# Kernel optimization log

Measured on AMD Instinct MI355X. Metric: run time of the kernel, lower is better.

## Reference

```python
import jax, jax.numpy as jnp
import numpy as np

N = 50000      # nodes
E = 800000     # edges (before self-loops)
F_IN = 256     # feature_size
H = 96         # hidden_channels
G = 64         # graphs in batch
NC = 4         # num_classes
EPS = 1e-5     # BatchNorm eps


def _lrelu(x, s=0.01):
    return jnp.where(x >= 0, x, s * x)


def _gat(x, W, a_s, a_d, b, src, dst):
    # PyG GATConv, heads=1: linear transform, edge-wise LeakyReLU(0.2) scores,
    # segment softmax over destination nodes, scatter-add aggregation.
    h = x @ W                                                  # [N,H]
    e = _lrelu((h * a_s).sum(-1)[src] + (h * a_d).sum(-1)[dst], 0.2)  # [E+N]
    m = jax.ops.segment_max(e, dst, num_segments=N)
    ee = jnp.exp(e - m[dst])
    denom = jax.ops.segment_sum(ee, dst, num_segments=N)
    alpha = ee / denom[dst]
    return jax.ops.segment_sum(alpha[:, None] * h[src], dst, num_segments=N) + b


def _bn(x, g, b):
    # training-mode BatchNorm over the node dimension
    mu = x.mean(0)
    var = ((x - mu) ** 2).mean(0)
    return g * (x - mu) / jnp.sqrt(var + EPS) + b


def setup_inputs() -> dict:
    key = jax.random.key(0)
    ks = jax.random.split(key, 20)
    p = lambda i, sh: jax.random.normal(ks[i], sh, jnp.float32) * 0.05
    inp = {
        "x": jax.random.normal(ks[0], (N, F_IN), jnp.float32),
        "edge_index": jax.random.randint(ks[1], (2, E), 0, N),
        "batch": jnp.sort(jax.random.randint(ks[2], (N,), 0, G)),
        "embed_W": p(3, (F_IN, H)), "embed_b": jnp.zeros((H,), jnp.float32),
        "conv1_W": p(4, (H, H)), "conv1_as": p(5, (H,)), "conv1_ad": p(6, (H,)), "conv1_b": jnp.zeros((H,), jnp.float32),
        "conv2_W": p(7, (H, H)), "conv2_as": p(8, (H,)), "conv2_ad": p(9, (H,)), "conv2_b": jnp.zeros((H,), jnp.float32),
        "conv3_W": p(10, (H, H)), "conv3_as": p(11, (H,)), "conv3_ad": p(12, (H,)), "conv3_b": jnp.zeros((H,), jnp.float32),
        "fc1_W": p(13, (H, H)), "fc1_b": jnp.zeros((H,), jnp.float32),
        "fc2_W": p(14, (H, H)), "fc2_b": jnp.zeros((H,), jnp.float32),
        "bn1_g": jnp.ones((H,), jnp.float32), "bn1_b": jnp.zeros((H,), jnp.float32),
        "bn2_g": jnp.ones((H,), jnp.float32), "bn2_b": jnp.zeros((H,), jnp.float32),
        "bn3_g": jnp.ones((H,), jnp.float32), "bn3_b": jnp.zeros((H,), jnp.float32),
        "fc3_W": p(15, (H, H // 2)), "fc3_b": jnp.zeros((H // 2,), jnp.float32),
        "fc4_W": p(16, (H // 2, NC)), "fc4_b": jnp.zeros((NC,), jnp.float32),
    }
    return inp


def reference(x, edge_index, batch, embed_W, embed_b,
              conv1_W, conv1_as, conv1_ad, conv1_b,
              conv2_W, conv2_as, conv2_ad, conv2_b,
              conv3_W, conv3_as, conv3_ad, conv3_b,
              fc1_W, fc1_b, fc2_W, fc2_b,
              bn1_g, bn1_b, bn2_g, bn2_b, bn3_g, bn3_b,
              fc3_W, fc3_b, fc4_W, fc4_b):
    loops = jnp.arange(N)
    src = jnp.concatenate([edge_index[0], loops])   # GATConv add_self_loops=True
    dst = jnp.concatenate([edge_index[1], loops])

    h = _lrelu(x @ embed_W + embed_b)
    identity = h
    h = _lrelu(_bn(_gat(h, conv1_W, conv1_as, conv1_ad, conv1_b, src, dst), bn1_g, bn1_b)) + identity
    h = _lrelu(h @ fc1_W + fc1_b)
    h = _lrelu(_bn(_gat(h, conv2_W, conv2_as, conv2_ad, conv2_b, src, dst), bn2_g, bn2_b)) + identity
    h = _lrelu(h @ fc2_W + fc2_b)
    h = _lrelu(_bn(_gat(h, conv3_W, conv3_as, conv3_ad, conv3_b, src, dst), bn3_g, bn3_b)) + identity

    # Poincare ball expmap0 with c=1: tanh(||u||) * u / ||u||
    n = jnp.maximum(jnp.linalg.norm(h, axis=-1, keepdims=True), 1e-15)
    h = jnp.tanh(n) * h / n

    cnt = jax.ops.segment_sum(jnp.ones((N,), h.dtype), batch, num_segments=G)
    pooled = jax.ops.segment_sum(h, batch, num_segments=G) / jnp.maximum(cnt, 1.0)[:, None]

    o = _lrelu(pooled @ fc3_W + fc3_b)
    return o @ fc4_W + fc4_b
```

## Files before the change

### kernel.cpp

```cpp
#include <hip/hip_runtime.h>
#include <hip/hip_bf16.h>

#define DEVINL __device__ __forceinline__

constexpr int N_NODES = 50000;
constexpr int N_EDGES = 800000;
constexpr int F_IN    = 256;
constexpr int H       = 96;
constexpr int NG      = 64;
constexpr float BN_EPS = 1e-5f;
constexpr int SLOT    = 64;
constexpr int NREP    = 8;
constexpr int REPSZ   = NG * H + NG;

typedef short bf16x8 __attribute__((ext_vector_type(8)));
typedef float f32x4  __attribute__((ext_vector_type(4)));

DEVINL float bf2f(unsigned int u) {
    union { unsigned int i; float f; } c; c.i = u << 16; return c.f;
}
DEVINL unsigned short f2bf(float f) {
    union { float f; unsigned int i; } c; c.f = f;
    unsigned int x = c.i;
    return (unsigned short)((x + 0x7fffu + ((x >> 16) & 1u)) >> 16);
}
DEVINL float lrelu01(float v) { return v >= 0.f ? v : 0.01f * v; }
DEVINL float ldf(const void* p, size_t i, int f32) {
    return f32 ? ((const float*)p)[i] : bf2f(((const unsigned short*)p)[i]);
}

__global__ __launch_bounds__(256) void detect_fill_k(const unsigned short* __restrict__ x,
                                                     int* __restrict__ flag,
                                                     int* __restrict__ fill)
{
    if (blockIdx.x == 0 && threadIdx.x < 64) {
        int l = threadIdx.x;
        float f = bf2f(x[l]);
        bool huge = !(fabsf(f) <= 1e4f);
        unsigned long long m = __ballot(huge);
        if (l == 0) flag[0] = (__popcll(m) >= 8) ? 1 : 0;
    }
    int i = blockIdx.x * 256 + threadIdx.x;
    if (i < N_NODES) fill[i] = 0;
}

__global__ __launch_bounds__(256) void wpackall_k(
    const void* __restrict__ sE, const void* __restrict__ s0,
    const void* __restrict__ s1, const void* __restrict__ s2,
    const void* __restrict__ s3, const void* __restrict__ s4,
    const int* __restrict__ dflag,
    unsigned short* __restrict__ dE, unsigned short* __restrict__ d0,
    unsigned short* __restrict__ d1, unsigned short* __restrict__ d2,
    unsigned short* __restrict__ d3, unsigned short* __restrict__ d4)
{
    int b = blockIdx.x;
    const void* src; unsigned short* dst; int K, i0;
    if (b < 96) { src = sE; dst = dE; K = F_IN; i0 = b * 256; }
    else {
        int m = (b - 96) / 36, r = (b - 96) % 36;
        K = H; i0 = r * 256;
        if      (m == 0) { src = s0; dst = d0; }
        else if (m == 1) { src = s1; dst = d1; }
        else if (m == 2) { src = s2; dst = d2; }
        else if (m == 3) { src = s3; dst = d3; }
        else             { src = s4; dst = d4; }
    }
    int i = i0 + threadIdx.x;
    if (i >= K * 96) return;
    int c   = i / 3072;
    int rem = i - c * 3072;
    int t    = rem >> 9;
    int rem2 = rem & 511;
    int l = rem2 >> 3, j = rem2 & 7;
    int k = c * 32 + (l >> 4) * 8 + j;
    int n = t * 16 + (l & 15);
    if (dflag[0]) dst[i] = f2bf(((const float*)src)[k * 96 + n]);
    else          dst[i] = ((const unsigned short*)src)[k * 96 + n];
}

template<int EPI, int AWS, int SD, int ABN, int SCAT>
__global__ __launch_bounds__(256) void mgemm_k(
    const void* __restrict__ Ap, const unsigned short* __restrict__ Wpk,
    const void* __restrict__ bp, const int* __restrict__ dflag,
    unsigned short* __restrict__ out, unsigned short* __restrict__ out2,
    const void* __restrict__ as_, const void* __restrict__ ad_,
    float* __restrict__ s, float* __restrict__ d,
    const float* __restrict__ coefp, const unsigned short* __restrict__ idn,
    const int* __restrict__ ei, int* __restrict__ fill,
    unsigned short* __restrict__ colw, int e0, int e1, int ngb,
    int M, int K)
{
    if (SCAT && (int)blockIdx.x >= ngb) {
        int e = e0 + ((int)blockIdx.x - ngb) * 256 + threadIdx.x;
        if (e < e1) {
            int srcv = ei[e];
            int dstv = ei[N_EDGES + e];
            int p = atomicAdd(&fill[dstv], 1);
            if (p < SLOT) colw[(size_t)dstv * SLOT + p] = (unsigned short)srcv;
        }
        return;
    }

    const int f32  = AWS ? 0 : dflag[0];
    const int wf32 = dflag[0];
    const int l    = threadIdx.x & 63;
    const int wave = threadIdx.x >> 6;
    const int row0 = blockIdx.x * 64 + wave * 16;
    const int m    = l & 15;
    const int q    = l >> 4;
    const int arow = row0 + m;
    const bool aok = arow < M;

    f32x4 acc[6] = {};
    const int nch = K >> 5;
    const bf16x8* wp = (const bf16x8*)Wpk;

    for (int c = 0; c < nch; c++) {
        bf16x8 a = {};
        if (aok) {
            if (ABN) {
                const int f0 = c * 32 + q * 8;
                uint4 xu = *(const uint4*)((const unsigned short*)Ap + (size_t)arow * K + f0);
                uint4 iu = *(const uint4*)(idn + (size_t)arow * K + f0);
                unsigned int xs[4] = { xu.x, xu.y, xu.z, xu.w };
                unsigned int is[4] = { iu.x, iu.y, iu.z, iu.w };
                #pragma unroll
                for (int jj = 0; jj < 4; jj++) {
                    int f = f0 + 2 * jj;
                    float v0 = lrelu01(bf2f(xs[jj] & 0xffff) * coefp[f]     + coefp[96 + f])     + bf2f(is[jj] & 0xffff);
                    float v1 = lrelu01(bf2f(xs[jj] >> 16)    * coefp[f + 1] + coefp[96 + f + 1]) + bf2f(is[jj] >> 16);
                    a[2 * jj]     = (short)f2bf(v0);
                    a[2 * jj + 1] = (short)f2bf(v1);
                }
            } else if (f32) {
                const float* A = (const float*)Ap + (size_t)arow * K + c * 32 + q * 8;
                #pragma unroll
                for (int j = 0; j < 8; j++) a[j] = (short)f2bf(A[j]);
            } else {
                a = *(const bf16x8*)((const unsigned short*)Ap + (size_t)arow * K + c * 32 + q * 8);
            }
        }
        const int base = c * 384 + l;
        #pragma unroll
        for (int t = 0; t < 6; t++)
            acc[t] = __builtin_amdgcn_mfma_f32_16x16x32_bf16(a, wp[base + t * 64], acc[t], 0, 0, 0);
    }

    float bv[6];
    if (EPI > 0) {
        #pragma unroll
        for (int t = 0; t < 6; t++) bv[t] = ldf(bp, t * 16 + m, wf32);
    }
    #pragma unroll
    for (int r = 0; r < 4; r++) {
        int rr = row0 + q * 4 + r;
        if (rr >= M) continue;
        size_t o = (size_t)rr * 96 + m;
        #pragma unroll
        for (int t = 0; t < 6; t++) {
            float v = acc[t][r];
            if (EPI > 0) v = lrelu01(v + bv[t]);
            unsigned short sv = f2bf(v);
            out[o + t * 16] = sv;
            if (EPI == 2) out2[o + t * 16] = sv;
        }
    }

    if (SD) {
        float asv[6], adv[6];
        #pragma unroll
        for (int t = 0; t < 6; t++) {
            asv[t] = ldf(as_, t * 16 + m, wf32);
            adv[t] = ldf(ad_, t * 16 + m, wf32);
        }
        #pragma unroll
        for (int r = 0; r < 4; r++) {
            float ps = 0.f, pd = 0.f;
            #pragma unroll
            for (int t = 0; t < 6; t++) {
                ps = fmaf(acc[t][r], asv[t], ps);
                pd = fmaf(acc[t][r], adv[t], pd);
            }
            #pragma unroll
            for (int off = 1; off < 16; off <<= 1) {
                ps += __shfl_xor(ps, off);
                pd += __shfl_xor(pd, off);
            }
            int rr = row0 + q * 4 + r;
            if (m == 0 && rr < M) { s[rr] = ps; d[rr] = pd; }
        }
    }
}

__global__ __launch_bounds__(256) void agg_k(
    const unsigned short* __restrict__ h2, const float* __restrict__ s,
    const float* __restrict__ d, const int* __restrict__ fill,
    const unsigned short* __restrict__ col, const void* __restrict__ bias,
    const int* __restrict__ dflag, unsigned short* __restrict__ out,
    float* __restrict__ bnsum, float* __restrict__ zp, int M)
{
    __shared__ uint2 uwb[4][80];
    if (blockIdx.x == 0 && threadIdx.x < 192) bnsum[threadIdx.x] = 0.f;
    if (zp) {
        int zi = blockIdx.x * 256 + threadIdx.x;
        if (zi < NREP * REPSZ) zp[zi] = 0.f;
    }
    int f32 = dflag[0];
    int v = (blockIdx.x * blockDim.x + threadIdx.x) >> 6;
    int l = threadIdx.x & 63;
    int wv = threadIdx.x >> 6;
    if (v >= M) return;
    int st   = v * SLOT;
    int degr = min(fill[v], SLOT - 1);
    int deg  = degr + 1;

    float dv = d[v];
    int u = 0; float e = -1e30f;
    if (l < degr) {
        u = col[st + l];
        float t = s[u] + dv;
        e = t >= 0.f ? t : 0.2f * t;
    } else if (l == degr) {
        u = v;
        float t = s[v] + dv;
        e = t >= 0.f ? t : 0.2f * t;
    }
    float lm = e;
    #pragma unroll
    for (int off = 32; off > 0; off >>= 1) lm = fmaxf(lm, __shfl_xor(lm, off));
    float w = (l < deg) ? __expf(e - lm) : 0.f;
    float ls = w;
    #pragma unroll
    for (int off = 32; off > 0; off >>= 1) ls += __shfl_xor(ls, off);
    float rden = 1.0f / ls;

    uwb[wv][l] = make_uint2((unsigned int)u, __float_as_uint(w));
    if (l < 16) uwb[wv][64 + l] = make_uint2(0u, 0u);

    bool hw = (l < 48);
    int  c2 = 2 * l;
    float a0 = 0.f, a1 = 0.f;
    const uint2* myuw = uwb[wv];
    for (int j = 0; j < deg; j += 16) {
        uint2 p[16];
        #pragma unroll
        for (int k = 0; k < 16; k++) p[k] = myuw[j + k];
        if (hw) {
            unsigned int hv[16];
            #pragma unroll
            for (int k = 0; k < 16; k++)
                hv[k] = *(const unsigned int*)(h2 + (size_t)p[k].x * 96 + c2);
            #pragma unroll
            for (int k = 0; k < 16; k++) {
                float wj = __uint_as_float(p[k].y);
                a0 = fmaf(wj, bf2f(hv[k] & 0xffff), a0);
                a1 = fmaf(wj, bf2f(hv[k] >> 16),    a1);
            }
        }
    }
    if (hw) {
        float b0 = ldf(bias, c2,     f32);
        float b1 = ldf(bias, c2 + 1, f32);
        unsigned int o = (unsigned int)f2bf(a0 * rden + b0)
                       | ((unsigned int)f2bf(a1 * rden + b1) << 16);
        *(unsigned int*)(out + (size_t)v * 96 + c2) = o;
    }
}

__global__ __launch_bounds__(192) void bnstats_k(const unsigned short* __restrict__ x,
                                                 float* __restrict__ sums, int M)
{
    int c  = threadIdx.x % 96;
    int g2 = threadIdx.x / 96;
    float s = 0.f, q = 0.f;
    for (int r = blockIdx.x * 2 + g2; r < M; r += gridDim.x * 2) {
        float v = bf2f(x[(size_t)r * 96 + c]);
        s += v; q += v * v;
    }
    __shared__ float lsd[192], lqd[192];
    lsd[threadIdx.x] = s; lqd[threadIdx.x] = q;
    __syncthreads();
    if (g2 == 0) {
        atomicAdd(&sums[c],      s + lsd[threadIdx.x + 96]);
        atomicAdd(&sums[96 + c], q + lqd[threadIdx.x + 96]);
    }
}

__global__ void bncoef_k(const float* __restrict__ sums,
                         const void* __restrict__ g_,
                         const void* __restrict__ b_,
                         const int* __restrict__ dflag,
                         float* __restrict__ coef)
{
    int c = threadIdx.x;
    if (c >= 96) return;
    int f32 = dflag[0];
    float mu  = sums[c] * (1.f / N_NODES);
    float var = sums[96 + c] * (1.f / N_NODES) - mu * mu;
    float rinv = 1.0f / sqrtf(var + BN_EPS);
    float sc = ldf(g_, c, f32) * rinv;
    coef[c]      = sc;
    coef[96 + c] = ldf(b_, c, f32) - mu * sc;
}

__global__ __launch_bounds__(256) void bnpool_k(
    const unsigned short* __restrict__ h, const float* __restrict__ coef,
    const unsigned short* __restrict__ iden, const int* __restrict__ batch,
    float* __restrict__ pooled8, int M)
{
    int w = (blockIdx.x * blockDim.x + threadIdx.x) >> 6;
    int l = threadIdx.x & 63;
    int v0 = w * 16;
    if (v0 >= M) return;
    float* P = pooled8 + (blockIdx.x & (NREP - 1)) * REPSZ;
    float* C = P + NG * H;
    bool hw = (l < 48);
    int  c2 = 2 * l;
    float sc0 = 0.f, sc1 = 0.f, sh0 = 0.f, sh1 = 0.f;
    if (hw) {
        sc0 = coef[c2]; sc1 = coef[c2 + 1];
        sh0 = coef[96 + c2]; sh1 = coef[97 + c2];
    }
    int nv = min(16, M - v0);

    int gb[16];
    #pragma unroll
    for (int k = 0; k < 16; k++) gb[k] = batch[v0 + min(k, nv - 1)];

    float x0[16], x1[16], q[16];
    #pragma unroll
    for (int k = 0; k < 16; k++) { x0[k] = 0.f; x1[k] = 0.f; q[k] = 0.f; }
    if (hw) {
        unsigned int xu[16], iu[16];
        #pragma unroll
        for (int k = 0; k < 16; k++) {
            int v = v0 + k;
            if (k < nv) {
                xu[k] = *(const unsigned int*)(h    + (size_t)v * 96 + c2);
                iu[k] = *(const unsigned int*)(iden + (size_t)v * 96 + c2);
            } else { xu[k] = 0u; iu[k] = 0u; }
        }
        #pragma unroll
        for (int k = 0; k < 16; k++) {
            x0[k] = lrelu01(bf2f(xu[k] & 0xffff) * sc0 + sh0) + bf2f(iu[k] & 0xffff);
            x1[k] = lrelu01(bf2f(xu[k] >> 16)    * sc1 + sh1) + bf2f(iu[k] >> 16);
            q[k]  = x0[k] * x0[k] + x1[k] * x1[k];
        }
    }

    #pragma unroll
    for (int off = 32; off > 0; off >>= 1) {
        #pragma unroll
        for (int k = 0; k < 16; k++) q[k] += __shfl_xor(q[k], off);
    }

    float f[16];
    #pragma unroll
    for (int k = 0; k < 16; k++) {
        float n = fmaxf(sqrtf(q[k]), 1e-15f);
        if (n < 15.f) {
            float t = __expf(2.f * n);
            f[k] = (t - 1.f) / ((t + 1.f) * n);
        } else {
            f[k] = 1.f / n;
        }
    }

    float a0 = 0.f, a1 = 0.f, cnt = 0.f;
    int curg = -1;
    for (int k = 0; k < nv; k++) {
        int g = gb[k];
        if (g != curg) {
            if (curg >= 0) {
                if (hw) {
                    atomicAdd(&P[curg * 96 + c2],     a0);
                    atomicAdd(&P[curg * 96 + c2 + 1], a1);
                }
                if (l == 0) atomicAdd(&C[curg], cnt);
            }
            a0 = a1 = 0.f; cnt = 0.f; curg = g;
        }
        a0 = fmaf(f[k], x0[k], a0);
        a1 = fmaf(f[k], x1[k], a1);
        cnt += 1.f;
    }
    if (curg >= 0) {
        if (hw) {
            atomicAdd(&P[curg * 96 + c2],     a0);
            atomicAdd(&P[curg * 96 + c2 + 1], a1);
        }
        if (l == 0) atomicAdd(&C[curg], cnt);
    }
}

__global__ __launch_bounds__(64) void head_k(const float* __restrict__ pooled8,
                                             const void* __restrict__ w3,
                                             const void* __restrict__ b3,
                                             const void* __restrict__ w4,
                                             const void* __restrict__ b4,
                                             const int* __restrict__ dflag,
                                             void* __restrict__ outv)
{
    int g = blockIdx.x;
    int t = threadIdx.x;
    int f32 = dflag[0];
    __shared__ float p[96];
    __shared__ float o[48];
    float cs = 0.f;
    #pragma unroll
    for (int r = 0; r < NREP; r++) cs += pooled8[r * REPSZ + NG * H + g];
    float inv = 1.0f / fmaxf(cs, 1.0f);
    for (int c = t; c < 96; c += 64) {
        float v = 0.f;
        #pragma unroll
        for (int r = 0; r < NREP; r++) v += pooled8[r * REPSZ + g * 96 + c];
        p[c] = v * inv;
    }
    __syncthreads();
    if (t < 48) {
        float a = ldf(b3, t, f32);
        #pragma unroll
        for (int c = 0; c < 96; c++) a = fmaf(p[c], ldf(w3, (size_t)c * 48 + t, f32), a);
        o[t] = lrelu01(a);
    }
    __syncthreads();
    if (t < 4) {
        float a = ldf(b4, t, f32);
        #pragma unroll
        for (int j = 0; j < 48; j++) a = fmaf(o[j], ldf(w4, j * 4 + t, f32), a);
        if (f32) ((float*)outv)[g * 4 + t] = a;
        else     ((unsigned short*)outv)[g * 4 + t] = f2bf(a);
    }
}

extern "C" void kernel_launch(void* const* d_in, const int* in_sizes, int n_in,
                              void* d_out, int out_size, void* d_ws, size_t ws_size,
                              hipStream_t stream)
{
    const void* x     = d_in[0];
    const int*  ei    = (const int*)d_in[1];
    const int*  batch = (const int*)d_in[2];
    const void* embW  = d_in[3];
    const void* embB  = d_in[4];
    const void* convW[3]  = { d_in[5],  d_in[9],  d_in[13] };
    const void* convAs[3] = { d_in[6],  d_in[10], d_in[14] };
    const void* convAd[3] = { d_in[7],  d_in[11], d_in[15] };
    const void* convB[3]  = { d_in[8],  d_in[12], d_in[16] };
    const void* fcW[2]    = { d_in[17], d_in[19] };
    const void* fcB[2]    = { d_in[18], d_in[20] };
    const void* bnG[3]    = { d_in[21], d_in[23], d_in[25] };
    const void* bnB[3]    = { d_in[22], d_in[24], d_in[26] };
    const void* fc3W = d_in[27];
    const void* fc3b = d_in[28];
    const void* fc4W = d_in[29];
    const void* fc4b = d_in[30];

    char* wp_ = (char*)d_ws;
    auto alloc = [&](size_t b) { char* p = wp_; wp_ += (b + 255) & ~(size_t)255; return p; };
    int*   dflag = (int*)alloc(256);
    unsigned short* ident = (unsigned short*)alloc((size_t)N_NODES * H * 2);
    unsigned short* hA    = (unsigned short*)alloc((size_t)N_NODES * H * 2);
    unsigned short* hB    = (unsigned short*)alloc((size_t)N_NODES * H * 2);
    float* s_sc  = (float*)alloc((size_t)N_NODES * 4);
    float* d_sc  = (float*)alloc((size_t)N_NODES * 4);
    float* bnsum = (float*)alloc(192 * 4);
    float* coef  = (float*)alloc(192 * 4);
    float* pooled8 = (float*)alloc((size_t)NREP * REPSZ * 4);
    int*   fill  = (int*)alloc((size_t)N_NODES * 4);
    unsigned short* col = (unsigned short*)alloc((size_t)N_NODES * SLOT * 2);
    unsigned short* wpkEmb = (unsigned short*)alloc((size_t)F_IN * 96 * 2);
    unsigned short* wpkS[5];
    for (int i = 0; i < 5; i++) wpkS[i] = (unsigned short*)alloc((size_t)H * 96 * 2);

    const int GM = (N_NODES + 63) / 64;
    const int GW = (N_NODES * 64 + 255) / 256;
    const int GP = ((N_NODES + 15) / 16 * 64 + 255) / 256;
    const int GF = (N_NODES + 255) / 256;
    const int EH = N_EDGES / 2;
    const int GS = (EH + 255) / 256;

    detect_fill_k<<<GF, 256, 0, stream>>>((const unsigned short*)x, dflag, fill);

    wpackall_k<<<276, 256, 0, stream>>>(embW, convW[0], convW[1], convW[2], fcW[0], fcW[1],
                                        dflag, wpkEmb, wpkS[0], wpkS[1], wpkS[2], wpkS[3], wpkS[4]);

    mgemm_k<2, 0, 0, 0, 1><<<GM + GS, 256, 0, stream>>>(
        x, wpkEmb, embB, dflag, hA, ident,
        nullptr, nullptr, nullptr, nullptr, nullptr, nullptr,
        ei, fill, col, 0, EH, GM, N_NODES, F_IN);

    unsigned short* hcur = hA;
    unsigned short* htmp = hB;

    for (int l = 0; l < 3; l++) {
        if (l == 0) {
            mgemm_k<0, 1, 1, 0, 1><<<GM + GS, 256, 0, stream>>>(
                hcur, wpkS[0], nullptr, dflag, htmp, nullptr,
                convAs[0], convAd[0], s_sc, d_sc, nullptr, nullptr,
                ei, fill, col, EH, N_EDGES, GM, N_NODES, H);
        } else {
            mgemm_k<0, 1, 1, 0, 0><<<GM, 256, 0, stream>>>(
                hcur, wpkS[l], nullptr, dflag, htmp, nullptr,
                convAs[l], convAd[l], s_sc, d_sc, nullptr, nullptr,
                nullptr, nullptr, nullptr, 0, 0, GM, N_NODES, H);
        }
        agg_k<<<GW, 256, 0, stream>>>(htmp, s_sc, d_sc, fill, col, convB[l], dflag, hcur,
                                      bnsum, (l == 2) ? pooled8 : nullptr, N_NODES);
        bnstats_k<<<512, 192, 0, stream>>>(hcur, bnsum, N_NODES);
        bncoef_k<<<1, 128, 0, stream>>>(bnsum, bnG[l], bnB[l], dflag, coef);
        if (l < 2) {
            mgemm_k<1, 1, 0, 1, 0><<<GM, 256, 0, stream>>>(
                hcur, wpkS[3 + l], fcB[l], dflag, htmp, nullptr,
                nullptr, nullptr, nullptr, nullptr, coef, ident,
                nullptr, nullptr, nullptr, 0, 0, GM, N_NODES, H);
            unsigned short* t = hcur; hcur = htmp; htmp = t;
        }
    }

    bnpool_k<<<GP, 256, 0, stream>>>(hcur, coef, ident, batch, pooled8, N_NODES);
    head_k<<<NG, 64, 0, stream>>>(pooled8, fc3W, fc3b, fc4W, fc4b, dflag, d_out);
}
```

Measured before the change: 436.2 us.

## Stage packed weights in LDS, preload A chunks, batch edge scatter per thread

The GEMM kernel now takes K as a template parameter, copies the packed weight matrix into shared memory once per block, and preloads every A chunk into registers before running the MFMA loop. The edge-scatter blocks each handle 8 edges per thread so that loads and atomics are batched. The embedding GEMM writes only to ident (EPI 1), dropping the duplicate hA output, and layer 0 reads from ident. The cost is more LDS per block (48KB for K=256) and more register pressure, which may lower occupancy.

```diff
diff --git a/kernel.cpp b/kernel.cpp
--- a/kernel.cpp
+++ b/kernel.cpp
@@ -12,6 +12,8 @@
 constexpr int SLOT    = 64;
 constexpr int NREP    = 8;
 constexpr int REPSZ   = NG * H + NG;
+constexpr int EPB     = 8;
+constexpr int ECHUNK  = 256 * EPB;
 
 typedef short bf16x8 __attribute__((ext_vector_type(8)));
 typedef float f32x4  __attribute__((ext_vector_type(4)));
@@ -78,7 +80,7 @@
     else          dst[i] = ((const unsigned short*)src)[k * 96 + n];
 }
 
-template<int EPI, int AWS, int SD, int ABN, int SCAT>
+template<int EPI, int AWS, int SD, int ABN, int SCAT, int K>
 __global__ __launch_bounds__(256) void mgemm_k(
     const void* __restrict__ Ap, const unsigned short* __restrict__ Wpk,
     const void* __restrict__ bp, const int* __restrict__ dflag,
@@ -88,18 +90,40 @@
     const float* __restrict__ coefp, const unsigned short* __restrict__ idn,
     const int* __restrict__ ei, int* __restrict__ fill,
     unsigned short* __restrict__ colw, int e0, int e1, int ngb,
-    int M, int K)
-{
+    int M)
+{
+    constexpr int NCH = K / 32;
+    __shared__ unsigned short Wlds[K * 96];
+
     if (SCAT && (int)blockIdx.x >= ngb) {
-        int e = e0 + ((int)blockIdx.x - ngb) * 256 + threadIdx.x;
-        if (e < e1) {
-            int srcv = ei[e];
-            int dstv = ei[N_EDGES + e];
-            int p = atomicAdd(&fill[dstv], 1);
-            if (p < SLOT) colw[(size_t)dstv * SLOT + p] = (unsigned short)srcv;
-        }
+        int b0 = e0 + ((int)blockIdx.x - ngb) * ECHUNK + (int)threadIdx.x;
+        int sv[EPB], dv[EPB];
+        bool ok[EPB];
+        #pragma unroll
+        for (int j = 0; j < EPB; j++) {
+            int e = b0 + j * 256;
+            ok[j] = (e < e1);
+            int ee = ok[j] ? e : e0;
+            sv[j] = ei[ee];
+            dv[j] = ei[N_EDGES + ee];
+        }
+        int p[EPB];
+        #pragma unroll
+        for (int j = 0; j < EPB; j++)
+            p[j] = ok[j] ? atomicAdd(&fill[dv[j]], 1) : SLOT;
+        #pragma unroll
+        for (int j = 0; j < EPB; j++)
+            if (p[j] < SLOT) colw[(size_t)dv[j] * SLOT + p[j]] = (unsigned short)sv[j];
         return;
     }
+
+    {
+        const uint4* ws = (const uint4*)Wpk;
+        uint4* wd = (uint4*)Wlds;
+        #pragma unroll 4
+        for (int i = threadIdx.x; i < K * 12; i += 256) wd[i] = ws[i];
+    }
+    __syncthreads();
 
     const int f32  = AWS ? 0 : dflag[0];
     const int wf32 = dflag[0];
@@ -111,11 +135,9 @@
     const int arow = row0 + m;
     const bool aok = arow < M;
 
-    f32x4 acc[6] = {};
-    const int nch = K >> 5;
-    const bf16x8* wp = (const bf16x8*)Wpk;
-
-    for (int c = 0; c < nch; c++) {
+    bf16x8 av[NCH];
+    #pragma unroll
+    for (int c = 0; c < NCH; c++) {
         bf16x8 a = {};
         if (aok) {
             if (ABN) {
@@ -140,10 +162,17 @@
                 a = *(const bf16x8*)((const unsigned short*)Ap + (size_t)arow * K + c * 32 + q * 8);
             }
         }
+        av[c] = a;
+    }
+
+    f32x4 acc[6] = {};
+    const bf16x8* wl = (const bf16x8*)Wlds;
+    #pragma unroll
+    for (int c = 0; c < NCH; c++) {
         const int base = c * 384 + l;
         #pragma unroll
         for (int t = 0; t < 6; t++)
-            acc[t] = __builtin_amdgcn_mfma_f32_16x16x32_bf16(a, wp[base + t * 64], acc[t], 0, 0, 0);
+            acc[t] = __builtin_amdgcn_mfma_f32_16x16x32_bf16(av[c], wl[base + t * 64], acc[t], 0, 0, 0);
     }
 
     float bv[6];
@@ -477,42 +506,42 @@
     const int GP = ((N_NODES + 15) / 16 * 64 + 255) / 256;
     const int GF = (N_NODES + 255) / 256;
     const int EH = N_EDGES / 2;
-    const int GS = (EH + 255) / 256;
+    const int GS = (EH + ECHUNK - 1) / ECHUNK;
 
     detect_fill_k<<<GF, 256, 0, stream>>>((const unsigned short*)x, dflag, fill);
 
     wpackall_k<<<276, 256, 0, stream>>>(embW, convW[0], convW[1], convW[2], fcW[0], fcW[1],
                                         dflag, wpkEmb, wpkS[0], wpkS[1], wpkS[2], wpkS[3], wpkS[4]);
 
-    mgemm_k<2, 0, 0, 0, 1><<<GM + GS, 256, 0, stream>>>(
-        x, wpkEmb, embB, dflag, hA, ident,
+    mgemm_k<1, 0, 0, 0, 1, F_IN><<<GM + GS, 256, 0, stream>>>(
+        x, wpkEmb, embB, dflag, ident, nullptr,
         nullptr, nullptr, nullptr, nullptr, nullptr, nullptr,
-        ei, fill, col, 0, EH, GM, N_NODES, F_IN);
+        ei, fill, col, 0, EH, GM, N_NODES);
 
     unsigned short* hcur = hA;
     unsigned short* htmp = hB;
 
     for (int l = 0; l < 3; l++) {
         if (l == 0) {
-            mgemm_k<0, 1, 1, 0, 1><<<GM + GS, 256, 0, stream>>>(
-                hcur, wpkS[0], nullptr, dflag, htmp, nullptr,
+            mgemm_k<0, 1, 1, 0, 1, H><<<GM + GS, 256, 0, stream>>>(
+                ident, wpkS[0], nullptr, dflag, htmp, nullptr,
                 convAs[0], convAd[0], s_sc, d_sc, nullptr, nullptr,
-                ei, fill, col, EH, N_EDGES, GM, N_NODES, H);
+                ei, fill, col, EH, N_EDGES, GM, N_NODES);
         } else {
-            mgemm_k<0, 1, 1, 0, 0><<<GM, 256, 0, stream>>>(
+            mgemm_k<0, 1, 1, 0, 0, H><<<GM, 256, 0, stream>>>(
                 hcur, wpkS[l], nullptr, dflag, htmp, nullptr,
                 convAs[l], convAd[l], s_sc, d_sc, nullptr, nullptr,
-                nullptr, nullptr, nullptr, 0, 0, GM, N_NODES, H);
+                nullptr, nullptr, nullptr, 0, 0, GM, N_NODES);
         }
         agg_k<<<GW, 256, 0, stream>>>(htmp, s_sc, d_sc, fill, col, convB[l], dflag, hcur,
                                       bnsum, (l == 2) ? pooled8 : nullptr, N_NODES);
         bnstats_k<<<512, 192, 0, stream>>>(hcur, bnsum, N_NODES);
         bncoef_k<<<1, 128, 0, stream>>>(bnsum, bnG[l], bnB[l], dflag, coef);
         if (l < 2) {
-            mgemm_k<1, 1, 0, 1, 0><<<GM, 256, 0, stream>>>(
+            mgemm_k<1, 1, 0, 1, 0, H><<<GM, 256, 0, stream>>>(
                 hcur, wpkS[3 + l], fcB[l], dflag, htmp, nullptr,
                 nullptr, nullptr, nullptr, nullptr, coef, ident,
-                nullptr, nullptr, nullptr, 0, 0, GM, N_NODES, H);
+                nullptr, nullptr, nullptr, 0, 0, GM, N_NODES);
             unsigned short* t = hcur; hcur = htmp; htmp = t;
         }
     }
```

Result: faster. 427.6 us (-2.0%).
